# Kernel tuning notes

Hardware: AMD Instinct MI355X
Metric: run time of the kernel (lower is better)

The kernel has to match this reference:

```python
import jax, jax.numpy as jnp
import numpy as np

B, T, D, E, H, A, P, V, N = 64, 600, 512, 640, 1024, 1024, 1024, 10025, 64
ZH, ZC = 0.05, 0.05  # zoneout probs (eval: deterministic interpolation)


def setup_inputs() -> dict:
    key = jax.random.key(0)
    ks = jax.random.split(key, 18)
    def init(k, shape, fan_in):
        return jax.random.normal(k, shape, jnp.float32) / np.sqrt(fan_in)
    return {
        "encoder_outputs": jax.random.normal(ks[0], (B, T, D), jnp.float32),
        "labels": jax.random.randint(ks[1], (B, N), 0, V),
        "enc_seq_len": jax.random.randint(ks[2], (B,), 300, T + 1),
        "embed": init(ks[3], (V, E), 1.0) * 0.1,          # embedding table
        "W_ih": init(ks[4], (4 * H, E + D), E + D),        # LSTMCell input weights (i,f,g,o)
        "b_ih": init(ks[5], (4 * H,), H),
        "b_hh": init(ks[6], (4 * H,), H),
        "W_s": init(ks[7], (A, H), H),                     # s_transformed (no bias)
        "W_enc": init(ks[8], (A, D), D),                   # enc_ctx
        "b_enc": init(ks[9], (A,), D),
        "v_att": init(ks[10], (A,), A),                    # attention energy vector
        "W_fert": init(ks[11], (D,), D),                   # inv_fertility (no bias)
        "W_fb": init(ks[12], (A,), 1.0),                   # weight_feedback: Linear(1, A)
        "W_r": init(ks[13], (P, H + E + D), H + E + D),    # readout_in
        "b_r": init(ks[14], (P,), P),
        "W_o": init(ks[15], (V, P // 2), P // 2),          # output proj
        "b_o": init(ks[16], (V,), V),
    }


def reference(encoder_outputs, labels, enc_seq_len, embed, W_ih, b_ih, b_hh,
              W_s, W_enc, b_enc, v_att, W_fert, W_fb, W_r, b_r, W_o, b_o):
    # shifted target embeddings: pad zero in front, drop last  [B,N,E]
    emb = embed[labels]
    emb = jnp.pad(emb, ((0, 0), (1, 0), (0, 0)))[:, :-1, :]

    enc_ctx = encoder_outputs @ W_enc.T + b_enc                       # [B,T,A]
    inv_fert = jax.nn.sigmoid(encoder_outputs @ W_fert)               # [B,T]
    mask = jnp.arange(T)[None, :] < enc_seq_len[:, None]              # [B,T]
    bias = b_ih + b_hh

    def step(carry, emb_t):
        h, c, ctx, accum = carry                                      # accum: [B,T]
        x = jnp.concatenate([emb_t, ctx], axis=-1)                    # [B,E+D]
        # NOTE: source calls cell(inputs) with NO state -> LSTMCell uses zero h,c
        gates = x @ W_ih.T + bias                                     # [B,4H]
        i, f, g, o = jnp.split(gates, 4, axis=-1)
        c_new = jax.nn.sigmoid(i) * jnp.tanh(g)                       # f * 0 + i * g
        h_new = jax.nn.sigmoid(o) * jnp.tanh(c_new)
        h = ZH * h + (1.0 - ZH) * h_new                               # zoneout (eval)
        c = ZC * c + (1.0 - ZC) * c_new
        q = h @ W_s.T                                                 # [B,A]
        fb = accum[..., None] * W_fb[None, None, :]                   # [B,T,A]
        e = jnp.tanh(enc_ctx + q[:, None, :] + fb) @ v_att            # [B,T]
        e = jnp.where(mask, e, -jnp.inf)
        w = jax.nn.softmax(e, axis=1)                                 # [B,T]
        ctx = jnp.einsum('bt,btd->bd', w, encoder_outputs)            # [B,D]
        accum = accum + w * inv_fert * 0.5
        return (h, c, ctx, accum), (h, ctx)

    zeros_h = jnp.zeros((B, H), encoder_outputs.dtype)
    carry0 = (zeros_h, zeros_h,
              jnp.zeros((B, D), encoder_outputs.dtype),
              jnp.zeros((B, T), encoder_outputs.dtype))
    _, (s_seq, ctx_seq) = jax.lax.scan(step, carry0, jnp.swapaxes(emb, 0, 1))
    s = jnp.swapaxes(s_seq, 0, 1)                                     # [B,N,H]
    ctx_s = jnp.swapaxes(ctx_seq, 0, 1)                               # [B,N,D]

    r = jnp.concatenate([s, emb, ctx_s], axis=-1) @ W_r.T + b_r       # [B,N,P]
    r = r.reshape(B, N, P // 2, 2).max(axis=-1)                       # maxout(2)
    logits = r @ W_o.T + b_o                                          # [B,N,V]
    return logits
```

## Files before the change

kernel.cpp:

```cpp
#include <hip/hip_runtime.h>
#include <math.h>

constexpr int cB = 64, cT = 600, cD = 512, cE = 640, cH = 1024, cA = 1024,
              cP = 1024, cV = 10025, cN = 64;
constexpr int cBT = cB * cT;
constexpr int cKr = cH + cE + cD;
constexpr int cM  = cB * cN;
constexpr int cVp = 10112;
constexpr int cG3 = 3 * cH;
constexpr int cTE = cT / 8;
constexpr int cXCS = 516;
constexpr int cNB = 8;

typedef __attribute__((ext_vector_type(8))) short bf16x8;
typedef __attribute__((ext_vector_type(4))) float f32x4;

__device__ __forceinline__ float bfu(unsigned short s) {
  return __uint_as_float(((unsigned int)s) << 16);
}
__device__ __forceinline__ unsigned short f2bf(float f) {
  unsigned int x = __float_as_uint(f);
  x += 0x7fffu + ((x >> 16) & 1u);
  return (unsigned short)(x >> 16);
}
__device__ __forceinline__ float fsig(float x) { return 1.0f / (1.0f + __expf(-x)); }
__device__ __forceinline__ float ftanh(float x) {
  float e = __expf(2.0f * x);
  return 1.0f - 2.0f / (e + 1.0f);
}

#define GLD(g, s)                                                          \
  __builtin_amdgcn_global_load_lds(                                       \
      (const __attribute__((address_space(1))) void*)(g),                 \
      (__attribute__((address_space(3))) void*)(s), 16, 0, 0)

__device__ __forceinline__ int xcd_swizzle(int bid, int nwg) {
  int q = nwg >> 3, r = nwg & 7;
  int x = bid & 7, loc = bid >> 3;
  return (x < r ? x * (q + 1) : r * (q + 1) + (x - r) * q) + loc;
}

__device__ __forceinline__ void ast(float* p, float v) {
  __hip_atomic_store(p, v, __ATOMIC_RELAXED, __HIP_MEMORY_SCOPE_AGENT);
}
__device__ __forceinline__ float ald(const float* p) {
  return __hip_atomic_load(p, __ATOMIC_RELAXED, __HIP_MEMORY_SCOPE_AGENT);
}
__device__ __forceinline__ void arrive_wait(unsigned* c, unsigned target) {
  __syncthreads();
  if (threadIdx.x == 0) {
    __hip_atomic_fetch_add(c, 1u, __ATOMIC_RELEASE, __HIP_MEMORY_SCOPE_AGENT);
    while (__hip_atomic_load(c, __ATOMIC_ACQUIRE, __HIP_MEMORY_SCOPE_AGENT) < target)
      __builtin_amdgcn_s_sleep(2);
  }
  __syncthreads();
}


__global__ __launch_bounds__(256) void cast_kernel(const float* __restrict__ in,
                                                   unsigned short* __restrict__ out) {
  int i = blockIdx.x * 256 + threadIdx.x;
  float4 v = reinterpret_cast<const float4*>(in)[i];
  ushort4 o;
  o.x = f2bf(v.x); o.y = f2bf(v.y); o.z = f2bf(v.z); o.w = f2bf(v.w);
  reinterpret_cast<ushort4*>(out)[i] = o;
}

__global__ __launch_bounds__(256) void cast_hl_kernel(const float* __restrict__ in,
                                                      unsigned short* __restrict__ hi,
                                                      unsigned short* __restrict__ lo) {
  int i = blockIdx.x * 256 + threadIdx.x;
  float4 v = reinterpret_cast<const float4*>(in)[i];
  ushort4 h, l;
  h.x = f2bf(v.x); h.y = f2bf(v.y); h.z = f2bf(v.z); h.w = f2bf(v.w);
  l.x = f2bf(v.x - bfu(h.x)); l.y = f2bf(v.y - bfu(h.y));
  l.z = f2bf(v.z - bfu(h.z)); l.w = f2bf(v.w - bfu(h.w));
  reinterpret_cast<ushort4*>(hi)[i] = h;
  reinterpret_cast<ushort4*>(lo)[i] = l;
}

__global__ __launch_bounds__(256) void cast_wo_kernel(const float* __restrict__ in,
                                                      unsigned short* __restrict__ hi,
                                                      unsigned short* __restrict__ lo) {
  int idx = blockIdx.x * 256 + threadIdx.x;
  int row = idx >> 7;
  int k = (idx & 127) * 4;
  float4 v = (row < cV) ? *reinterpret_cast<const float4*>(&in[(size_t)row * cD + k])
                        : make_float4(0.f, 0.f, 0.f, 0.f);
  ushort4 h, l;
  h.x = f2bf(v.x); h.y = f2bf(v.y); h.z = f2bf(v.z); h.w = f2bf(v.w);
  l.x = f2bf(v.x - bfu(h.x)); l.y = f2bf(v.y - bfu(h.y));
  l.z = f2bf(v.z - bfu(h.z)); l.w = f2bf(v.w - bfu(h.w));
  reinterpret_cast<ushort4*>(hi)[idx] = h;
  reinterpret_cast<ushort4*>(lo)[idx] = l;
}

__global__ __launch_bounds__(256) void fert_kernel(const float* __restrict__ enc,
                                                   const float* __restrict__ W_fert,
                                                   float* __restrict__ inv_fert) {
  int wave = threadIdx.x >> 6, lane = threadIdx.x & 63;
  int row = blockIdx.x * 4 + wave;
  const float* r = enc + (size_t)row * cD;
  float s = 0.0f;
#pragma unroll
  for (int i = 0; i < 8; ++i) s += r[lane + 64 * i] * W_fert[lane + 64 * i];
#pragma unroll
  for (int o = 32; o; o >>= 1) s += __shfl_xor(s, o);
  if (lane == 0) inv_fert[row] = 1.0f / (1.0f + __expf(-s));
}

__global__ __launch_bounds__(256) void build_aemb(const float* __restrict__ embed,
                                                  const int* __restrict__ labels,
                                                  unsigned short* __restrict__ Ah,
                                                  unsigned short* __restrict__ Al) {
  int idx = blockIdx.x * 256 + threadIdx.x;
  int row = idx / (cE / 4);
  int k = (idx % (cE / 4)) * 4;
  int b = row >> 6, tt = row & 63;
  float4 v = make_float4(0.f, 0.f, 0.f, 0.f);
  if (tt > 0) {
    int lab = labels[b * cN + tt - 1];
    v = *reinterpret_cast<const float4*>(&embed[(size_t)lab * cE + k]);
  }
  ushort4 h, l;
  h.x = f2bf(v.x); h.y = f2bf(v.y); h.z = f2bf(v.z); h.w = f2bf(v.w);
  l.x = f2bf(v.x - bfu(h.x)); l.y = f2bf(v.y - bfu(h.y));
  l.z = f2bf(v.z - bfu(h.z)); l.w = f2bf(v.w - bfu(h.w));
  *reinterpret_cast<ushort4*>(&Ah[(size_t)row * cE + k]) = h;
  *reinterpret_cast<ushort4*>(&Al[(size_t)row * cE + k]) = l;
}

__global__ __launch_bounds__(256) void cast_wihe(const float* __restrict__ W_ih,
                                                 unsigned short* __restrict__ Wh,
                                                 unsigned short* __restrict__ Wl) {
  int idx = blockIdx.x * 256 + threadIdx.x;
  int jcol = idx / (cE / 4);
  int k = (idx % (cE / 4)) * 4;
  int r = (jcol < cH) ? jcol : jcol + cH;
  float4 v = *reinterpret_cast<const float4*>(&W_ih[(size_t)r * (cE + cD) + k]);
  ushort4 h, l;
  h.x = f2bf(v.x); h.y = f2bf(v.y); h.z = f2bf(v.z); h.w = f2bf(v.w);
  l.x = f2bf(v.x - bfu(h.x)); l.y = f2bf(v.y - bfu(h.y));
  l.z = f2bf(v.z - bfu(h.z)); l.w = f2bf(v.w - bfu(h.w));
  *reinterpret_cast<ushort4*>(&Wh[(size_t)jcol * cE + k]) = h;
  *reinterpret_cast<ushort4*>(&Wl[(size_t)jcol * cE + k]) = l;
}

__global__ __launch_bounds__(256) void pack_wih(const float* __restrict__ W_ih,
                                                unsigned short* __restrict__ WihP) {
  int idx = blockIdx.x * 256 + threadIdx.x;
  int col = idx >> 7;
  int k4 = idx & 127;
  int r = (col < cH) ? col : col + cH;
  float4 v = *reinterpret_cast<const float4*>(&W_ih[(size_t)r * (cE + cD) + cE + k4 * 4]);
  ushort4 h;
  h.x = f2bf(v.x); h.y = f2bf(v.y); h.z = f2bf(v.z); h.w = f2bf(v.w);
  *reinterpret_cast<ushort4*>(&WihP[((size_t)k4 * cG3 + col) * 4]) = h;
}

__global__ __launch_bounds__(256) void pack_ws(const float* __restrict__ W_s,
                                               unsigned short* __restrict__ WsP) {
  int idx = blockIdx.x * 256 + threadIdx.x;
  int a = idx >> 8;
  int k4 = idx & 255;
  float4 v = *reinterpret_cast<const float4*>(&W_s[(size_t)a * cH + k4 * 4]);
  ushort4 h;
  h.x = f2bf(v.x); h.y = f2bf(v.y); h.z = f2bf(v.z); h.w = f2bf(v.w);
  *reinterpret_cast<ushort4*>(&WsP[((size_t)k4 * cA + a) * 4]) = h;
}

__global__ __launch_bounds__(256) void build_ar_kernel(
    const float* __restrict__ s_seq, const float* __restrict__ ctx_seq,
    const float* __restrict__ embed, const int* __restrict__ labels,
    unsigned short* __restrict__ Ah, unsigned short* __restrict__ Al) {
  int idx = blockIdx.x * 256 + threadIdx.x;
  int row = idx / (cKr / 4);
  int k = (idx % (cKr / 4)) * 4;
  int b = row >> 6, tt = row & 63;
  float4 v;
  if (k < cH) {
    v = *reinterpret_cast<const float4*>(&s_seq[(size_t)row * cH + k]);
  } else if (k < cH + cE) {
    if (tt == 0) {
      v = make_float4(0.f, 0.f, 0.f, 0.f);
    } else {
      int lab = labels[b * cN + tt - 1];
      v = *reinterpret_cast<const float4*>(&embed[(size_t)lab * cE + (k - cH)]);
    }
  } else {
    v = *reinterpret_cast<const float4*>(&ctx_seq[(size_t)row * cD + (k - cH - cE)]);
  }
  ushort4 h, l;
  h.x = f2bf(v.x); h.y = f2bf(v.y); h.z = f2bf(v.z); h.w = f2bf(v.w);
  l.x = f2bf(v.x - bfu(h.x)); l.y = f2bf(v.y - bfu(h.y));
  l.z = f2bf(v.z - bfu(h.z)); l.w = f2bf(v.w - bfu(h.w));
  *reinterpret_cast<ushort4*>(&Ah[(size_t)row * cKr + k]) = h;
  *reinterpret_cast<ushort4*>(&Al[(size_t)row * cKr + k]) = l;
}


__global__ __launch_bounds__(256) void mfma_encctx(const unsigned short* __restrict__ A,
                                                   const unsigned short* __restrict__ Bm,
                                                   const float* __restrict__ bias,
                                                   unsigned short* __restrict__ C) {
  __shared__ unsigned short sA[4096], sB[4096];
  constexpr int nbx = cA / 128;
  int bid = xcd_swizzle(blockIdx.x, gridDim.x);
  int by = bid / nbx, bx = bid % nbx;
  int tid = threadIdx.x;
  int w = tid >> 6, l = tid & 63;
  int m0 = by * 128, n0 = bx * 128;
  int wr = w >> 1, wc = w & 1;
  f32x4 acc[4][4] = {};
  int srow = tid >> 2, scol = (tid & 3) * 8;
  for (int k0 = 0; k0 < cD; k0 += 32) {
    __syncthreads();
    GLD(&A[(size_t)(m0 + srow) * cD + k0 + scol], &sA[tid * 8]);
    GLD(&A[(size_t)(m0 + 64 + srow) * cD + k0 + scol], &sA[2048 + tid * 8]);
    GLD(&Bm[(size_t)(n0 + srow) * cD + k0 + scol], &sB[tid * 8]);
    GLD(&Bm[(size_t)(n0 + 64 + srow) * cD + k0 + scol], &sB[2048 + tid * 8]);
    __syncthreads();
    int rA = wr * 64 + (l & 15);
    int rB = wc * 64 + (l & 15);
    int kg = (l >> 4) * 8;
    bf16x8 a[4], b[4];
#pragma unroll
    for (int i = 0; i < 4; ++i) a[i] = *(const bf16x8*)&sA[(rA + i * 16) * 32 + kg];
#pragma unroll
    for (int j = 0; j < 4; ++j) b[j] = *(const bf16x8*)&sB[(rB + j * 16) * 32 + kg];
#pragma unroll
    for (int i = 0; i < 4; ++i)
#pragma unroll
      for (int j = 0; j < 4; ++j)
        acc[i][j] = __builtin_amdgcn_mfma_f32_16x16x32_bf16(a[i], b[j], acc[i][j], 0, 0, 0);
  }
  int rbase = m0 + wr * 64 + ((l >> 4) * 4);
  int cbase = n0 + wc * 64 + (l & 15);
  float bv[4];
#pragma unroll
  for (int j = 0; j < 4; ++j) bv[j] = bias[cbase + j * 16];
#pragma unroll
  for (int i = 0; i < 4; ++i)
#pragma unroll
    for (int q = 0; q < 4; ++q) {
      int row = rbase + i * 16 + q;
#pragma unroll
      for (int j = 0; j < 4; ++j) {
        int col = cbase + j * 16;
        int pos = (col < 512) ? (2 * col) : (2 * (col - 512) + 1);
        C[(size_t)row * cA + pos] = f2bf(acc[i][j][q] + bv[j]);
      }
    }
}

template <int EP>
__global__ __launch_bounds__(256) void mfma_gemm3(
    const unsigned short* __restrict__ Ah, const unsigned short* __restrict__ Al,
    const unsigned short* __restrict__ Bh, const unsigned short* __restrict__ Bl,
    const float* __restrict__ bias, void* __restrict__ outv, int K, int nbx) {
  __shared__ unsigned short sAh[4096], sAl[4096], sBh[4096], sBl[4096];
  int bid = xcd_swizzle(blockIdx.x, gridDim.x);
  int by = bid / nbx, bx = bid % nbx;
  int tid = threadIdx.x;
  int w = tid >> 6, l = tid & 63;
  int m0 = by * 128, n0 = bx * 128;
  int wr = w >> 1, wc = w & 1;
  f32x4 acc[4][4] = {};
  int srow = tid >> 2, scol = (tid & 3) * 8;
  for (int k0 = 0; k0 < K; k0 += 32) {
    __syncthreads();
    GLD(&Ah[(size_t)(m0 + srow) * K + k0 + scol], &sAh[tid * 8]);
    GLD(&Ah[(size_t)(m0 + 64 + srow) * K + k0 + scol], &sAh[2048 + tid * 8]);
    GLD(&Al[(size_t)(m0 + srow) * K + k0 + scol], &sAl[tid * 8]);
    GLD(&Al[(size_t)(m0 + 64 + srow) * K + k0 + scol], &sAl[2048 + tid * 8]);
    GLD(&Bh[(size_t)(n0 + srow) * K + k0 + scol], &sBh[tid * 8]);
    GLD(&Bh[(size_t)(n0 + 64 + srow) * K + k0 + scol], &sBh[2048 + tid * 8]);
    GLD(&Bl[(size_t)(n0 + srow) * K + k0 + scol], &sBl[tid * 8]);
    GLD(&Bl[(size_t)(n0 + 64 + srow) * K + k0 + scol], &sBl[2048 + tid * 8]);
    __syncthreads();
    int rA = wr * 64 + (l & 15);
    int rB = wc * 64 + (l & 15);
    int kg = (l >> 4) * 8;
    bf16x8 bh[4], bl[4];
#pragma unroll
    for (int j = 0; j < 4; ++j) {
      bh[j] = *(const bf16x8*)&sBh[(rB + j * 16) * 32 + kg];
      bl[j] = *(const bf16x8*)&sBl[(rB + j * 16) * 32 + kg];
    }
#pragma unroll
    for (int i = 0; i < 4; ++i) {
      bf16x8 ah = *(const bf16x8*)&sAh[(rA + i * 16) * 32 + kg];
      bf16x8 al = *(const bf16x8*)&sAl[(rA + i * 16) * 32 + kg];
#pragma unroll
      for (int j = 0; j < 4; ++j) {
        acc[i][j] = __builtin_amdgcn_mfma_f32_16x16x32_bf16(ah, bh[j], acc[i][j], 0, 0, 0);
        acc[i][j] = __builtin_amdgcn_mfma_f32_16x16x32_bf16(ah, bl[j], acc[i][j], 0, 0, 0);
        acc[i][j] = __builtin_amdgcn_mfma_f32_16x16x32_bf16(al, bh[j], acc[i][j], 0, 0, 0);
        if (EP == 2)
          acc[i][j] = __builtin_amdgcn_mfma_f32_16x16x32_bf16(al, bl[j], acc[i][j], 0, 0, 0);
      }
    }
  }
  int rbase = m0 + wr * 64 + ((l >> 4) * 4);
  int cbase = n0 + wc * 64 + (l & 15);
  if (EP == 0) {
    unsigned short* mo_h = (unsigned short*)outv;
    unsigned short* mo_l = mo_h + (size_t)cM * (cP / 2);
#pragma unroll
    for (int i = 0; i < 4; ++i)
#pragma unroll
      for (int q = 0; q < 4; ++q) {
        int row = rbase + i * 16 + q;
#pragma unroll
        for (int j = 0; j < 4; ++j) {
          float v = acc[i][j][q] + bias[cbase + j * 16];
          float o = fmaxf(v, __shfl_xor(v, 1));
          if (!(l & 1)) {
            int ch = (cbase + j * 16) >> 1;
            unsigned short h = f2bf(o);
            mo_h[(size_t)row * (cP / 2) + ch] = h;
            mo_l[(size_t)row * (cP / 2) + ch] = f2bf(o - bfu(h));
          }
        }
      }
  } else if (EP == 1) {
    float* out = (float*)outv;
#pragma unroll
    for (int i = 0; i < 4; ++i)
#pragma unroll
      for (int q = 0; q < 4; ++q) {
        int row = rbase + i * 16 + q;
#pragma unroll
        for (int j = 0; j < 4; ++j) {
          int col = cbase + j * 16;
          if (col < cV) out[(size_t)row * cV + col] = acc[i][j][q] + bias[col];
        }
      }
  } else {
    float* out = (float*)outv;
#pragma unroll
    for (int i = 0; i < 4; ++i)
#pragma unroll
      for (int q = 0; q < 4; ++q) {
        int row = rbase + i * 16 + q;
#pragma unroll
        for (int j = 0; j < 4; ++j)
          out[(size_t)row * cG3 + cbase + j * 16] = acc[i][j][q];
      }
  }
}


struct LoopArgs {
  const unsigned short* enc_ctx;
  const unsigned short* enc_bf;
  const unsigned short* WihP;
  const unsigned short* WsP;
  const float* b_ih;
  const float* b_hh;
  const float* embg;
  const float* inv_fert;
  const float* v_att;
  const float* W_fb;
  const int* slen;
  float* s_seq;
  float* ctx_seq;
  float* xq;
  float* xc;
  unsigned* cnt;
};

__global__ __launch_bounds__(1024, 8)
void split_loop(LoopArgs A) {
  __shared__ float ctx_s[cD];
  __shared__ float h_s[128];
  __shared__ float q_s[cA];
  __shared__ float ew_s[cTE + 5];
  __shared__ float acc_s[cTE];
  __shared__ float fert_s[cTE];
  __shared__ float vatt_s[cA];
  __shared__ float wfb_s[cA];
  __shared__ float cpartL[4][256];
  __shared__ float cpartH[4][256];
  __shared__ float red_s[16];
  __shared__ float ms_s[16];

  const int od = blockIdx.x & 7;
  const int b = blockIdx.x >> 3;
  const int tid = threadIdx.x;
  const int wv = tid >> 6, ln = tid & 63;
  const int jl = tid >> 3, part = tid & 7;
  const int gp = tid >> 8, pp = tid & 255;
  const int j0 = od * 128;
  const int len = A.slen[b];
  unsigned* cntQ = A.cnt + (0 * cB + b) * 64;
  unsigned* cntS = A.cnt + (1 * cB + b) * 64;

  if (tid < cD) ctx_s[tid] = 0.f;
  vatt_s[tid] = A.v_att[tid];
  wfb_s[tid] = A.W_fb[tid];
  if (tid < cTE) {
    acc_s[tid] = 0.f;
    fert_s[tid] = A.inv_fert[b * cT + 8 * tid + od];
  }
  if (tid >= cTE && tid < cTE + 5) ew_s[tid] = 0.f;
  float h_my = 0.f, bgi = 0.f, bgg = 0.f, bgo = 0.f;
  if (part == 0) {
    int j = j0 + jl;
    bgi = A.b_ih[j] + A.b_hh[j];
    bgg = A.b_ih[j + 2048] + A.b_hh[j + 2048];
    bgo = A.b_ih[j + 3072] + A.b_hh[j + 3072];
  }
  __syncthreads();

  for (int t = 0; t < cN; ++t) {
    const int par = t & 1;
    const unsigned tgt = (unsigned)cNB * (t + 1);

    {
      float ai = 0.f, ag = 0.f, ao = 0.f;
      const unsigned short* wbase = A.WihP + (size_t)(j0 + jl) * 4;
#pragma unroll 4
      for (int k4 = 0; k4 < 16; ++k4) {
        int kk = (k4 + 2 * part) & 15;
        int row = part * 16 + kk;
        float4 c = *reinterpret_cast<const float4*>(&ctx_s[row * 4]);
        const unsigned short* pw = wbase + (size_t)row * (cG3 * 4);
        ushort4 wi = *reinterpret_cast<const ushort4*>(pw);
        ushort4 wg = *reinterpret_cast<const ushort4*>(pw + (size_t)1024 * 4);
        ushort4 wo = *reinterpret_cast<const ushort4*>(pw + (size_t)2048 * 4);
        ai += bfu(wi.x) * c.x + bfu(wi.y) * c.y + bfu(wi.z) * c.z + bfu(wi.w) * c.w;
        ag += bfu(wg.x) * c.x + bfu(wg.y) * c.y + bfu(wg.z) * c.z + bfu(wg.w) * c.w;
        ao += bfu(wo.x) * c.x + bfu(wo.y) * c.y + bfu(wo.z) * c.z + bfu(wo.w) * c.w;
      }
      ai += __shfl_xor(ai, 1); ai += __shfl_xor(ai, 2); ai += __shfl_xor(ai, 4);
      ag += __shfl_xor(ag, 1); ag += __shfl_xor(ag, 2); ag += __shfl_xor(ag, 4);
      ao += __shfl_xor(ao, 1); ao += __shfl_xor(ao, 2); ao += __shfl_xor(ao, 4);
      if (part == 0) {
        int j = j0 + jl;
        const float* eg = A.embg + (size_t)(b * cN + t) * cG3;
        float gi = ai + bgi + eg[j];
        float gg = ag + bgg + eg[j + 1024];
        float go = ao + bgo + eg[j + 2048];
        float hnew = fsig(go) * ftanh(fsig(gi) * ftanh(gg));
        h_my = 0.05f * h_my + 0.95f * hnew;
        A.s_seq[(size_t)(b * cN + t) * cH + j] = h_my;
        h_s[jl] = h_my;
      }
    }
    __syncthreads();

    {
      float aq = 0.f;
      const unsigned short* pw = A.WsP + ((size_t)(od * 32) * cA + tid) * 4;
#pragma unroll 8
      for (int kk = 0; kk < 32; ++kk) {
        float4 hh = *reinterpret_cast<const float4*>(&h_s[kk * 4]);
        ushort4 w = *reinterpret_cast<const ushort4*>(pw);
        aq += bfu(w.x) * hh.x + bfu(w.y) * hh.y + bfu(w.z) * hh.z + bfu(w.w) * hh.w;
        pw += (size_t)cA * 4;
      }
      ast(&A.xq[(((size_t)par * cB + b) * cNB + od) * cA + tid], aq);
    }
    arrive_wait(cntQ, tgt);
    {
      const float* xb = A.xq + ((size_t)par * cB + b) * cNB * cA;
      float s = 0.f;
#pragma unroll
      for (int o = 0; o < cNB; ++o) s += ald(&xb[o * cA + tid]);
      q_s[tid] = s;
    }
    __syncthreads();

#pragma unroll
    for (int ip = 0; ip < 5; ++ip) {
      int i = wv + 16 * ip;
      if (ip == 4 && i >= cTE) continue;
      int tt = 8 * i + od;
      if (tt >= len) {
        if (ln == 0) ew_s[i] = -__builtin_inff();
        continue;
      }
      float fb = acc_s[i];
      const unsigned* rowp = (const unsigned*)(A.enc_ctx + (size_t)(b * cT + tt) * cA);
      float acc = 0.f;
#pragma unroll
      for (int k2 = 0; k2 < 8; ++k2) {
        unsigned u = rowp[ln + 64 * k2];
        int a0 = ln + 64 * k2;
        float c0 = __uint_as_float(u << 16);
        float c1 = __uint_as_float(u & 0xffff0000u);
        acc += vatt_s[a0] * ftanh(c0 + q_s[a0] + fb * wfb_s[a0]);
        acc += vatt_s[a0 + 512] * ftanh(c1 + q_s[a0 + 512] + fb * wfb_s[a0 + 512]);
      }
#pragma unroll
      for (int o = 32; o; o >>= 1) acc += __shfl_xor(acc, o);
      if (ln == 0) ew_s[i] = acc;
    }
    __syncthreads();

    float m_loc;
    {
      float m = (tid < cTE) ? ew_s[tid] : -__builtin_inff();
#pragma unroll
      for (int o = 32; o; o >>= 1) m = fmaxf(m, __shfl_xor(m, o));
      if (ln == 0) red_s[wv] = m;
      __syncthreads();
      m = red_s[0];
#pragma unroll
      for (int w2 = 1; w2 < 16; ++w2) m = fmaxf(m, red_s[w2]);
      m_loc = m;
      __syncthreads();
      float wn = 0.f;
      if (tid < cTE) {
        float e = ew_s[tid];
        if (e > -__builtin_inff()) wn = __expf(e - m_loc);
        ew_s[tid] = wn;
      }
      float sp = wn;
#pragma unroll
      for (int o = 32; o; o >>= 1) sp += __shfl_xor(sp, o);
      if (ln == 0) red_s[wv] = sp;
      __syncthreads();
    }
    float s_loc = red_s[0];
#pragma unroll
    for (int w2 = 1; w2 < 16; ++w2) s_loc += red_s[w2];
    __syncthreads();

    {
      float s0 = 0.f, s1 = 0.f;
#pragma unroll
      for (int ii = 0; ii < 19; ++ii) {
        int i = gp + 4 * ii;
        if (i < cTE) {
          float wgt = ew_s[i];
          unsigned u =
              ((const unsigned*)(A.enc_bf + ((size_t)b * cT + 8 * i + od) * cD))[pp];
          s0 += wgt * __uint_as_float(u << 16);
          s1 += wgt * __uint_as_float(u & 0xffff0000u);
        }
      }
      cpartL[gp][pp] = s0;
      cpartH[gp][pp] = s1;
    }
    __syncthreads();
    {
      float* xcb = A.xc + (((size_t)par * cB + b) * cNB + od) * cXCS;
      if (tid < cD) {
        int p2 = tid >> 1;
        float v = (tid & 1)
                      ? (cpartH[0][p2] + cpartH[1][p2] + cpartH[2][p2] + cpartH[3][p2])
                      : (cpartL[0][p2] + cpartL[1][p2] + cpartL[2][p2] + cpartL[3][p2]);
        ast(&xcb[2 + tid], v);
      }
      if (tid == 0) ast(&xcb[0], m_loc);
      if (tid == 1) ast(&xcb[1], s_loc);
    }
    arrive_wait(cntS, tgt);

    if (tid < 16) {
      ms_s[tid] =
          ald(&A.xc[(((size_t)par * cB + b) * cNB + (tid >> 1)) * cXCS + (tid & 1)]);
    }
    __syncthreads();
    {
      float M = -__builtin_inff();
#pragma unroll
      for (int o = 0; o < cNB; ++o) M = fmaxf(M, ms_s[2 * o]);
      float tot = 0.f;
      float sc[cNB];
#pragma unroll
      for (int o = 0; o < cNB; ++o) {
        sc[o] = __expf(ms_s[2 * o] - M);
        tot += ms_s[2 * o + 1] * sc[o];
      }
      float invt = 1.0f / tot;
      if (tid < cD) {
        const float* xcb = A.xc + ((size_t)par * cB + b) * cNB * cXCS;
        float cv = 0.f;
#pragma unroll
        for (int o = 0; o < cNB; ++o) cv += ald(&xcb[o * cXCS + 2 + tid]) * sc[o];
        cv *= invt;
        ctx_s[tid] = cv;
        if (od == 0) A.ctx_seq[(size_t)(b * cN + t) * cD + tid] = cv;
      } else {
        int i = tid - 512;
        if (i < cTE) {
          float scq = __expf(m_loc - M);
          acc_s[i] += ew_s[i] * scq * invt * fert_s[i] * 0.5f;
        }
      }
    }
    __syncthreads();
  }
}


extern "C" void kernel_launch(void* const* d_in, const int* in_sizes, int n_in,
                              void* d_out, int out_size, void* d_ws, size_t ws_size,
                              hipStream_t stream) {
  (void)in_sizes; (void)n_in; (void)out_size; (void)ws_size;
  const float* enc    = (const float*)d_in[0];
  const int*   labels = (const int*)d_in[1];
  const int*   slen   = (const int*)d_in[2];
  const float* embed  = (const float*)d_in[3];
  const float* W_ih   = (const float*)d_in[4];
  const float* b_ih   = (const float*)d_in[5];
  const float* b_hh   = (const float*)d_in[6];
  const float* W_s    = (const float*)d_in[7];
  const float* W_enc  = (const float*)d_in[8];
  const float* b_enc  = (const float*)d_in[9];
  const float* v_att  = (const float*)d_in[10];
  const float* W_fert = (const float*)d_in[11];
  const float* W_fb   = (const float*)d_in[12];
  const float* W_r    = (const float*)d_in[13];
  const float* b_r    = (const float*)d_in[14];
  const float* W_o    = (const float*)d_in[15];
  const float* b_o    = (const float*)d_in[16];
  float* out = (float*)d_out;

  char* ws = (char*)d_ws;
  size_t off = 0;
  auto alloc = [&](size_t bytes) -> char* {
    char* p = ws + off;
    off = (off + bytes + 255) & ~(size_t)255;
    return p;
  };
  unsigned short* enc_ctx = (unsigned short*)alloc((size_t)cBT * cA * 2);
  unsigned short* enc_bf  = (unsigned short*)alloc((size_t)cBT * cD * 2);
  unsigned short* wencb   = (unsigned short*)alloc((size_t)cA * cD * 2);
  float* inv_fert = (float*)alloc((size_t)cBT * 4);
  unsigned short* WihP = (unsigned short*)alloc((size_t)cD * cG3 * 2);
  unsigned short* WsP  = (unsigned short*)alloc((size_t)cH * cA * 2);
  float* embg     = (float*)alloc((size_t)cM * cG3 * 4);
  float* s_seq    = (float*)alloc((size_t)cM * cH * 4);
  float* ctx_seq  = (float*)alloc((size_t)cM * cD * 4);
  float* xq       = (float*)alloc((size_t)2 * cB * cNB * cA * 4);
  float* xc       = (float*)alloc((size_t)2 * cB * cNB * cXCS * 4);
  unsigned* cnt   = (unsigned*)alloc((size_t)2 * cB * 64 * 4);
  unsigned short* Aemb_h = (unsigned short*)alloc((size_t)cM * cE * 2);
  unsigned short* Aemb_l = (unsigned short*)alloc((size_t)cM * cE * 2);
  unsigned short* Wihe_h = (unsigned short*)alloc((size_t)cG3 * cE * 2);
  unsigned short* Wihe_l = (unsigned short*)alloc((size_t)cG3 * cE * 2);
  unsigned short* Ar_h = (unsigned short*)alloc((size_t)cM * cKr * 2);
  unsigned short* Ar_l = (unsigned short*)alloc((size_t)cM * cKr * 2);
  unsigned short* Wr_h = (unsigned short*)alloc((size_t)cP * cKr * 2);
  unsigned short* Wr_l = (unsigned short*)alloc((size_t)cP * cKr * 2);
  unsigned short* mo_hl = (unsigned short*)alloc((size_t)2 * cM * (cP / 2) * 2);
  unsigned short* Wo_h = (unsigned short*)alloc((size_t)cVp * cD * 2);
  unsigned short* Wo_l = (unsigned short*)alloc((size_t)cVp * cD * 2);

  hipMemsetAsync(cnt, 0, (size_t)2 * cB * 64 * 4, stream);

  cast_kernel<<<(cBT * cD) / 1024, 256, 0, stream>>>(enc, enc_bf);
  cast_kernel<<<(cA * cD) / 1024, 256, 0, stream>>>(W_enc, wencb);
  fert_kernel<<<cBT / 4, 256, 0, stream>>>(enc, W_fert, inv_fert);
  mfma_encctx<<<(cBT / 128) * (cA / 128), 256, 0, stream>>>(enc_bf, wencb, b_enc, enc_ctx);
  build_aemb<<<(cM * cE / 4) / 256, 256, 0, stream>>>(embed, labels, Aemb_h, Aemb_l);
  cast_wihe<<<(cG3 * cE / 4) / 256, 256, 0, stream>>>(W_ih, Wihe_h, Wihe_l);
  pack_wih<<<(cG3 * (cD / 4)) / 256, 256, 0, stream>>>(W_ih, WihP);
  pack_ws<<<(cA * (cH / 4)) / 256, 256, 0, stream>>>(W_s, WsP);
  cast_hl_kernel<<<(cP * cKr) / 1024, 256, 0, stream>>>(W_r, Wr_h, Wr_l);
  cast_wo_kernel<<<(cVp * cD) / 1024, 256, 0, stream>>>(W_o, Wo_h, Wo_l);
  mfma_gemm3<2><<<(cM / 128) * (cG3 / 128), 256, 0, stream>>>(
      Aemb_h, Aemb_l, Wihe_h, Wihe_l, nullptr, (void*)embg, cE, cG3 / 128);

  LoopArgs la;
  la.enc_ctx = enc_ctx; la.enc_bf = enc_bf; la.WihP = WihP; la.WsP = WsP;
  la.b_ih = b_ih; la.b_hh = b_hh; la.embg = embg; la.inv_fert = inv_fert;
  la.v_att = v_att; la.W_fb = W_fb; la.slen = slen;
  la.s_seq = s_seq; la.ctx_seq = ctx_seq;
  la.xq = xq; la.xc = xc; la.cnt = cnt;
  split_loop<<<dim3(cB * cNB), dim3(1024), 0, stream>>>(la);

  build_ar_kernel<<<(cM * cKr) / 1024, 256, 0, stream>>>(s_seq, ctx_seq, embed, labels,
                                                         Ar_h, Ar_l);
  mfma_gemm3<0><<<(cM / 128) * (cP / 128), 256, 0, stream>>>(Ar_h, Ar_l, Wr_h, Wr_l, b_r,
                                                             (void*)mo_hl, cKr, cP / 128);
  unsigned short* mo_h = mo_hl;
  unsigned short* mo_l = mo_hl + (size_t)cM * (cP / 2);
  mfma_gemm3<1><<<(cM / 128) * (cVp / 128), 256, 0, stream>>>(mo_h, mo_l, Wo_h, Wo_l, b_o,
                                                              (void*)out, cP / 2, cVp / 128);
}
```

Measured before the change: 7.598 ms.

## Double-buffer enc_ctx and encoder rows through LDS in attention loop

Stages the per-block encoder-context rows and bf16 encoder rows through a double-buffered shared-memory buffer using async global-to-LDS loads (GLD). The next chunk is prefetched while the current one is consumed, and the first chunk is issued before the cross-block barrier. The goal is to hide global memory latency in the attention-energy and context-sum phases of the recurrent loop. In exchange it uses 32 KB more LDS, adds a __syncthreads per chunk, and skips work for masked positions via nv.

```diff
diff --git a/kernel.cpp b/kernel.cpp
--- a/kernel.cpp
+++ b/kernel.cpp
@@ -384,6 +384,8 @@
   __shared__ float cpartH[4][256];
   __shared__ float red_s[16];
   __shared__ float ms_s[16];
+  __shared__ float rp2_s[2][8][2];
+  __shared__ unsigned short ec_s[2][8192];
 
   const int od = blockIdx.x & 7;
   const int b = blockIdx.x >> 3;
@@ -393,6 +395,7 @@
   const int gp = tid >> 8, pp = tid & 255;
   const int j0 = od * 128;
   const int len = A.slen[b];
+  const int nv = (len - od + 7) >> 3;
   unsigned* cntQ = A.cnt + (0 * cB + b) * 64;
   unsigned* cntS = A.cnt + (1 * cB + b) * 64;
 
@@ -462,6 +465,11 @@
       }
       ast(&A.xq[(((size_t)par * cB + b) * cNB + od) * cA + tid], aq);
     }
+    {
+      int r = tid >> 7;
+      size_t gr = (size_t)b * cT + (size_t)8 * r + od;
+      GLD(A.enc_ctx + gr * cA + (size_t)(tid & 127) * 8, &ec_s[0][tid * 8]);
+    }
     arrive_wait(cntQ, tgt);
     {
       const float* xb = A.xq + ((size_t)par * cB + b) * cNB * cA;
@@ -472,33 +480,50 @@
     }
     __syncthreads();
 
-#pragma unroll
-    for (int ip = 0; ip < 5; ++ip) {
-      int i = wv + 16 * ip;
-      if (ip == 4 && i >= cTE) continue;
-      int tt = 8 * i + od;
-      if (tt >= len) {
-        if (ln == 0) ew_s[i] = -__builtin_inff();
-        continue;
-      }
-      float fb = acc_s[i];
-      const unsigned* rowp = (const unsigned*)(A.enc_ctx + (size_t)(b * cT + tt) * cA);
-      float acc = 0.f;
-#pragma unroll
-      for (int k2 = 0; k2 < 8; ++k2) {
-        unsigned u = rowp[ln + 64 * k2];
-        int a0 = ln + 64 * k2;
-        float c0 = __uint_as_float(u << 16);
-        float c1 = __uint_as_float(u & 0xffff0000u);
-        acc += vatt_s[a0] * ftanh(c0 + q_s[a0] + fb * wfb_s[a0]);
-        acc += vatt_s[a0 + 512] * ftanh(c1 + q_s[a0 + 512] + fb * wfb_s[a0 + 512]);
-      }
-#pragma unroll
-      for (int o = 32; o; o >>= 1) acc += __shfl_xor(acc, o);
-      if (ln == 0) ew_s[i] = acc;
-    }
-    __syncthreads();
-
+    for (int c = 0; c < 10; ++c) {
+      const int cur = c & 1;
+      if (c < 9) {
+        int r = tid >> 7;
+        size_t gr = (size_t)b * cT + (size_t)8 * (8 * (c + 1) + r) + od;
+        if (gr >= (size_t)cBT) gr = (size_t)cBT - 1;
+        GLD(A.enc_ctx + gr * cA + (size_t)(tid & 127) * 8, &ec_s[cur ^ 1][tid * 8]);
+      }
+      {
+        int r = wv >> 1, hf = wv & 1;
+        int i = 8 * c + r;
+        float acc = 0.f;
+        if (i < nv) {
+          float fb = acc_s[i];
+          const unsigned* rp = (const unsigned*)&ec_s[cur][r * 1024];
+#pragma unroll
+          for (int k2 = 0; k2 < 4; ++k2) {
+            int a0 = hf * 256 + ln + 64 * k2;
+            unsigned u = rp[a0];
+            float c0 = __uint_as_float(u << 16);
+            float c1 = __uint_as_float(u & 0xffff0000u);
+            acc += vatt_s[a0] * ftanh(c0 + q_s[a0] + fb * wfb_s[a0]);
+            acc += vatt_s[a0 + 512] * ftanh(c1 + q_s[a0 + 512] + fb * wfb_s[a0 + 512]);
+          }
+#pragma unroll
+          for (int o = 32; o; o >>= 1) acc += __shfl_xor(acc, o);
+        }
+        if (ln == 0) rp2_s[cur][r][hf] = acc;
+      }
+      __syncthreads();
+      if (tid < 8) {
+        int i = 8 * c + tid;
+        if (i < cTE)
+          ew_s[i] = (i < nv) ? (rp2_s[cur][tid][0] + rp2_s[cur][tid][1])
+                             : -__builtin_inff();
+      }
+    }
+    __syncthreads();
+
+    {
+      int rr = tid >> 6;
+      size_t gr = (size_t)b * cT + (size_t)8 * rr + od;
+      GLD(A.enc_bf + gr * cD + (size_t)(tid & 63) * 8, &ec_s[0][tid * 8]);
+    }
     float m_loc;
     {
       float m = (tid < cTE) ? ew_s[tid] : -__builtin_inff();
@@ -530,16 +555,26 @@
 
     {
       float s0 = 0.f, s1 = 0.f;
-#pragma unroll
-      for (int ii = 0; ii < 19; ++ii) {
-        int i = gp + 4 * ii;
-        if (i < cTE) {
-          float wgt = ew_s[i];
-          unsigned u =
-              ((const unsigned*)(A.enc_bf + ((size_t)b * cT + 8 * i + od) * cD))[pp];
-          s0 += wgt * __uint_as_float(u << 16);
-          s1 += wgt * __uint_as_float(u & 0xffff0000u);
+      for (int c = 0; c < 5; ++c) {
+        const int cur = c & 1;
+        if (c < 4) {
+          int rr = tid >> 6;
+          size_t gr = (size_t)b * cT + (size_t)8 * (16 * (c + 1) + rr) + od;
+          if (gr >= (size_t)cBT) gr = (size_t)cBT - 1;
+          GLD(A.enc_bf + gr * cD + (size_t)(tid & 63) * 8, &ec_s[cur ^ 1][tid * 8]);
         }
+#pragma unroll
+        for (int l2 = 0; l2 < 4; ++l2) {
+          int lr = gp + 4 * l2;
+          int i = 16 * c + lr;
+          if (i < nv) {
+            float wgt = ew_s[i];
+            unsigned u = ((const unsigned*)&ec_s[cur][lr * 512])[pp];
+            s0 += wgt * __uint_as_float(u << 16);
+            s1 += wgt * __uint_as_float(u & 0xffff0000u);
+          }
+        }
+        __syncthreads();
       }
       cpartL[gp][pp] = s0;
       cpartH[gp][pp] = s1;
```

Result: faster. 7.270 ms (-4.3%).

## Prefetch enc_ctx and encoder rows into LDS with double-buffered async loads

Applied to the files above, without the earlier changes.

The attention-energy and context loops in the recurrent kernel now stage each wave's enc_ctx and encoder rows into a 64 KB shared buffer using async global-to-LDS loads (GLD), double-buffered with explicit s_waitcnt. The first row is issued before the inter-block barrier so the load overlaps the wait. Loop trip counts are derived from the sequence length, so masked rows past len are never loaded. The context reduction is reorganised to one row per wave with a 16-way cross-wave sum, reusing the big buffer. This hides global latency on the serial per-step path, at the cost of much more shared memory per block, which may reduce occupancy, and extra LDS traffic.

```diff
diff --git a/kernel.cpp b/kernel.cpp
--- a/kernel.cpp
+++ b/kernel.cpp
@@ -375,24 +375,24 @@
   __shared__ float ctx_s[cD];
   __shared__ float h_s[128];
   __shared__ float q_s[cA];
-  __shared__ float ew_s[cTE + 5];
+  __shared__ float ew_s[cTE];
   __shared__ float acc_s[cTE];
   __shared__ float fert_s[cTE];
   __shared__ float vatt_s[cA];
   __shared__ float wfb_s[cA];
-  __shared__ float cpartL[4][256];
-  __shared__ float cpartH[4][256];
   __shared__ float red_s[16];
   __shared__ float ms_s[16];
+  __shared__ __align__(16) unsigned short big_s[32768];
 
   const int od = blockIdx.x & 7;
   const int b = blockIdx.x >> 3;
   const int tid = threadIdx.x;
   const int wv = tid >> 6, ln = tid & 63;
   const int jl = tid >> 3, part = tid & 7;
-  const int gp = tid >> 8, pp = tid & 255;
   const int j0 = od * 128;
   const int len = A.slen[b];
+  const int nv = (len - od + 7) >> 3;
+  const int nr = (nv - wv + 15) >> 4;
   unsigned* cntQ = A.cnt + (0 * cB + b) * 64;
   unsigned* cntS = A.cnt + (1 * cB + b) * 64;
 
@@ -403,7 +403,6 @@
     acc_s[tid] = 0.f;
     fert_s[tid] = A.inv_fert[b * cT + 8 * tid + od];
   }
-  if (tid >= cTE && tid < cTE + 5) ew_s[tid] = 0.f;
   float h_my = 0.f, bgi = 0.f, bgg = 0.f, bgo = 0.f;
   if (part == 0) {
     int j = j0 + jl;
@@ -462,6 +461,12 @@
       }
       ast(&A.xq[(((size_t)par * cB + b) * cNB + od) * cA + tid], aq);
     }
+    {
+      const unsigned short* src = A.enc_ctx + ((size_t)b * cT + 8 * wv + od) * cA;
+      unsigned short* dst = &big_s[wv * 2048];
+      GLD(src + ln * 8, dst + ln * 8);
+      GLD(src + 512 + ln * 8, dst + 512 + ln * 8);
+    }
     arrive_wait(cntQ, tgt);
     {
       const float* xb = A.xq + ((size_t)par * cB + b) * cNB * cA;
@@ -472,21 +477,24 @@
     }
     __syncthreads();
 
-#pragma unroll
-    for (int ip = 0; ip < 5; ++ip) {
-      int i = wv + 16 * ip;
-      if (ip == 4 && i >= cTE) continue;
-      int tt = 8 * i + od;
-      if (tt >= len) {
-        if (ln == 0) ew_s[i] = -__builtin_inff();
-        continue;
-      }
+    for (int r = 0; r < nr; ++r) {
+      if (r + 1 < nr) {
+        int i2 = wv + 16 * (r + 1);
+        const unsigned short* src = A.enc_ctx + ((size_t)b * cT + 8 * i2 + od) * cA;
+        unsigned short* dst = &big_s[wv * 2048 + ((r + 1) & 1) * 1024];
+        GLD(src + ln * 8, dst + ln * 8);
+        GLD(src + 512 + ln * 8, dst + 512 + ln * 8);
+        asm volatile("s_waitcnt vmcnt(2)" ::: "memory");
+      } else {
+        asm volatile("s_waitcnt vmcnt(0)" ::: "memory");
+      }
+      int i = wv + 16 * r;
       float fb = acc_s[i];
-      const unsigned* rowp = (const unsigned*)(A.enc_ctx + (size_t)(b * cT + tt) * cA);
+      const unsigned* rp = (const unsigned*)&big_s[wv * 2048 + (r & 1) * 1024];
       float acc = 0.f;
 #pragma unroll
       for (int k2 = 0; k2 < 8; ++k2) {
-        unsigned u = rowp[ln + 64 * k2];
+        unsigned u = rp[ln + 64 * k2];
         int a0 = ln + 64 * k2;
         float c0 = __uint_as_float(u << 16);
         float c1 = __uint_as_float(u & 0xffff0000u);
@@ -497,7 +505,14 @@
       for (int o = 32; o; o >>= 1) acc += __shfl_xor(acc, o);
       if (ln == 0) ew_s[i] = acc;
     }
-    __syncthreads();
+    if (nv + tid < cTE) ew_s[nv + tid] = -__builtin_inff();
+    __syncthreads();
+
+    {
+      const unsigned short* src = A.enc_bf + ((size_t)b * cT + 8 * wv + od) * cD;
+      unsigned short* dst = &big_s[16384 + wv * 1024];
+      GLD(src + ln * 8, dst + ln * 8);
+    }
 
     float m_loc;
     {
@@ -529,29 +544,44 @@
     __syncthreads();
 
     {
-      float s0 = 0.f, s1 = 0.f;
-#pragma unroll
-      for (int ii = 0; ii < 19; ++ii) {
-        int i = gp + 4 * ii;
-        if (i < cTE) {
-          float wgt = ew_s[i];
-          unsigned u =
-              ((const unsigned*)(A.enc_bf + ((size_t)b * cT + 8 * i + od) * cD))[pp];
-          s0 += wgt * __uint_as_float(u << 16);
-          s1 += wgt * __uint_as_float(u & 0xffff0000u);
+      float s0[4] = {0.f, 0.f, 0.f, 0.f}, s1[4] = {0.f, 0.f, 0.f, 0.f};
+      for (int r = 0; r < nr; ++r) {
+        if (r + 1 < nr) {
+          int i2 = wv + 16 * (r + 1);
+          const unsigned short* src = A.enc_bf + ((size_t)b * cT + 8 * i2 + od) * cD;
+          unsigned short* dst = &big_s[16384 + wv * 1024 + ((r + 1) & 1) * 512];
+          GLD(src + ln * 8, dst + ln * 8);
+          asm volatile("s_waitcnt vmcnt(1)" ::: "memory");
+        } else {
+          asm volatile("s_waitcnt vmcnt(0)" ::: "memory");
         }
-      }
-      cpartL[gp][pp] = s0;
-      cpartH[gp][pp] = s1;
+        int i = wv + 16 * r;
+        float wgt = ew_s[i];
+        const unsigned* rp = (const unsigned*)&big_s[16384 + wv * 1024 + (r & 1) * 512];
+#pragma unroll
+        for (int k = 0; k < 4; ++k) {
+          unsigned u = rp[ln + 64 * k];
+          s0[k] += wgt * __uint_as_float(u << 16);
+          s1[k] += wgt * __uint_as_float(u & 0xffff0000u);
+        }
+      }
+      float2* cp = (float2*)big_s;
+#pragma unroll
+      for (int k = 0; k < 4; ++k)
+        cp[wv * 256 + ln + 64 * k] = make_float2(s0[k], s1[k]);
     }
     __syncthreads();
     {
       float* xcb = A.xc + (((size_t)par * cB + b) * cNB + od) * cXCS;
       if (tid < cD) {
-        int p2 = tid >> 1;
-        float v = (tid & 1)
-                      ? (cpartH[0][p2] + cpartH[1][p2] + cpartH[2][p2] + cpartH[3][p2])
-                      : (cpartL[0][p2] + cpartL[1][p2] + cpartL[2][p2] + cpartL[3][p2]);
+        const float2* cp = (const float2*)big_s;
+        int j = tid >> 1;
+        float v = 0.f;
+#pragma unroll
+        for (int w = 0; w < 16; ++w) {
+          float2 p = cp[w * 256 + j];
+          v += (tid & 1) ? p.y : p.x;
+        }
         ast(&xcb[2 + tid], v);
       }
       if (tid == 0) ast(&xcb[0], m_loc);
```

Measured after the change: 6.886 ms. -9.4%, faster.
